# Optimization experiments

Measured on AMD Instinct MI355X. Metric: run time of the kernel, lower is better.

Reference implementation:

```python
import jax, jax.numpy as jnp
import numpy as np
import math

HIDDEN = 1024
HEADS = 16
HEAD_DIM = HIDDEN // HEADS
B, S = 2, 2048


def setup_inputs() -> dict:
    key = jax.random.key(0)
    ks = jax.random.split(key, 10)
    std = 1.0 / math.sqrt(HIDDEN)
    mk = lambda k: (jax.random.normal(k, (HIDDEN, HIDDEN), jnp.float32) * std)
    return {
        "hidden_states": jax.random.normal(ks[0], (B, S, HIDDEN), jnp.float32),
        "attention_mask": jnp.zeros((B, 1, 1, S), jnp.float32),
        "wq": mk(ks[1]), "bq": jnp.zeros((HIDDEN,), jnp.float32),
        "wk": mk(ks[2]), "bk": jnp.zeros((HIDDEN,), jnp.float32),
        "wv": mk(ks[3]), "bv": jnp.zeros((HIDDEN,), jnp.float32),
        "wo": mk(ks[4]), "bo": jnp.zeros((HIDDEN,), jnp.float32),
    }


def reference(hidden_states, attention_mask, wq, bq, wk, bk, wv, bv, wo, bo):
    b, s, _ = hidden_states.shape
    scale = math.sqrt(HEAD_DIM)
    # projections (torch Linear: x @ W.T + b); weights stored as [out, in]
    q = hidden_states @ wq.T + bq
    k = hidden_states @ wk.T + bk
    v = hidden_states @ wv.T + bv
    # [B, H, S, D]
    q = q.reshape(b, s, HEADS, HEAD_DIM).transpose(0, 2, 1, 3)
    k = k.reshape(b, s, HEADS, HEAD_DIM).transpose(0, 2, 1, 3)
    v = v.reshape(b, s, HEADS, HEAD_DIM).transpose(0, 2, 1, 3)
    scores = jnp.einsum("bhqd,bhkd->bhqk", q, k) / scale
    scores = scores + attention_mask  # broadcast [B,1,1,S]
    weights = jax.nn.softmax(scores, axis=-1)  # dropout = identity (eval)
    out = jnp.einsum("bhqk,bhkd->bhqd", weights, v)
    out = out.transpose(0, 2, 1, 3).reshape(b, s, HIDDEN)
    out = out @ wo.T + bo
    return out
```

## Files before the change

kernel.cpp:

```cpp
#include <hip/hip_runtime.h>
#include <hip/hip_bf16.h>

typedef __bf16 bf16_t;
typedef __bf16 bf16x8 __attribute__((ext_vector_type(8)));
typedef _Float16 f16x4 __attribute__((ext_vector_type(4)));
typedef _Float16 f16x8 __attribute__((ext_vector_type(8)));
typedef float f32x4 __attribute__((ext_vector_type(4)));

#define SEQ    2048
#define NH     16
#define HD     64
#define HIDDEN 1024
#define LOG2E  1.44269504f
#define CSTR   41

__device__ __forceinline__ bf16_t to_bf16(float f) { return (bf16_t)f; }

__device__ __forceinline__ void async16(const void* g, void* l) {
    __builtin_amdgcn_global_load_lds((const __attribute__((address_space(1))) void*)g,
                                     (__attribute__((address_space(3))) void*)l, 16, 0, 0);
}

__global__ __launch_bounds__(256) void cvt_kernel(
    const float* __restrict__ s0, bf16_t* __restrict__ d0, int c0,
    const float* __restrict__ s1, bf16_t* __restrict__ d1, int c1,
    const float* __restrict__ s2, bf16_t* __restrict__ d2, int c2,
    const float* __restrict__ s3, bf16_t* __restrict__ d3, int c3,
    const float* __restrict__ s4, bf16_t* __restrict__ d4, int c4)
{
    int blk = blockIdx.x;
    const float* s; bf16_t* d;
    if (blk < c0)              { s = s0; d = d0; }
    else if ((blk -= c0) < c1) { s = s1; d = d1; }
    else if ((blk -= c1) < c2) { s = s2; d = d2; }
    else if ((blk -= c2) < c3) { s = s3; d = d3; }
    else                       { blk -= c3; s = s4; d = d4; }
    const size_t base = (size_t)blk * 2048 + threadIdx.x * 8;
    const float4 a = *(const float4*)&s[base];
    const float4 b = *(const float4*)&s[base + 4];
    bf16x8 o;
    o[0] = (bf16_t)a.x; o[1] = (bf16_t)a.y; o[2] = (bf16_t)a.z; o[3] = (bf16_t)a.w;
    o[4] = (bf16_t)b.x; o[5] = (bf16_t)b.y; o[6] = (bf16_t)b.z; o[7] = (bf16_t)b.w;
    *(bf16x8*)&d[base] = o;
}

__global__ __launch_bounds__(256, 3) void qkv_kernel(
    const bf16_t* __restrict__ X,
    const bf16_t* __restrict__ wq, const bf16_t* __restrict__ wk, const bf16_t* __restrict__ wv,
    const float* __restrict__ bq, const float* __restrict__ bk, const float* __restrict__ bv,
    bf16_t* __restrict__ qws, bf16_t* __restrict__ kws, _Float16* __restrict__ vws)
{
    __shared__ __align__(16) bf16_t Sh[2 * 128 * 64];
    bf16_t* As = Sh;
    bf16_t* Bs = Sh + 128 * 64;
    const int z = blockIdx.z;
    const bf16_t* Wsel = (z == 0) ? wq : (z == 1) ? wk : wv;
    const float*  bsel = (z == 0) ? bq : (z == 1) ? bk : bv;
    const int m0 = blockIdx.y * 128, n0 = blockIdx.x * 128;

    const int t = threadIdx.x, lane = t & 63, w = t >> 6;
    const int w0 = w & 1, w1 = w >> 1, l15 = lane & 15, q4 = lane >> 4;

    f32x4 acc[4][4];
#pragma unroll
    for (int i = 0; i < 4; i++)
#pragma unroll
        for (int j = 0; j < 4; j++) acc[i][j] = f32x4{0.f, 0.f, 0.f, 0.f};

    for (int kt = 0; kt < HIDDEN; kt += 64) {
#pragma unroll
        for (int j = 0; j < 4; j++) {
            const int s = j * 256 + t;
            const int row = s >> 3, c = (s & 7) ^ (row & 7);
            const int lbase = (j * 256 + w * 64) * 8;
            async16(&X[(size_t)(m0 + row) * HIDDEN + kt + c * 8], &As[lbase]);
            async16(&Wsel[(size_t)(n0 + row) * HIDDEN + kt + c * 8], &Bs[lbase]);
        }
        __syncthreads();
#pragma unroll
        for (int ks = 0; ks < 2; ks++) {
            bf16x8 af[4];
#pragma unroll
            for (int ti = 0; ti < 4; ti++) {
                const int ra = w0 * 64 + ti * 16 + l15;
                af[ti] = *(const bf16x8*)&As[ra * 64 + (((ks * 4 + q4) ^ (ra & 7))) * 8];
            }
#pragma unroll
            for (int tj = 0; tj < 4; tj++) {
                const int rb = w1 * 64 + tj * 16 + l15;
                const bf16x8 bfr = *(const bf16x8*)&Bs[rb * 64 + (((ks * 4 + q4) ^ (rb & 7))) * 8];
#pragma unroll
                for (int ti = 0; ti < 4; ti++)
                    acc[ti][tj] = __builtin_amdgcn_mfma_f32_16x16x32_bf16(af[ti], bfr, acc[ti][tj], 0, 0, 0);
            }
        }
        __syncthreads();
    }

    if (z < 2) {
#pragma unroll
        for (int tj = 0; tj < 4; tj++) {
            const int n = w1 * 64 + tj * 16 + l15;
            const float bb = bsel[n0 + n];
            const int ch = (n >> 3), sub = n & 7;
#pragma unroll
            for (int ti = 0; ti < 4; ti++)
#pragma unroll
                for (int r = 0; r < 4; r++) {
                    const int m = w0 * 64 + ti * 16 + q4 * 4 + r;
                    Sh[m * 128 + ((ch ^ (m & 15)) << 3) + sub] = to_bf16(acc[ti][tj][r] + bb);
                }
        }
        __syncthreads();
        bf16_t* dst = (z == 0) ? qws : kws;
#pragma unroll
        for (int i = 0; i < 8; i++) {
            const int g = i * 256 + t;
            const int row = g >> 4, c = g & 15;
            const bf16x8 vv = *(const bf16x8*)&Sh[row * 128 + ((c ^ (row & 15)) << 3)];
            *(bf16x8*)&dst[(size_t)(m0 + row) * HIDDEN + n0 + c * 8] = vv;
        }
    } else {
        _Float16* Vt = (_Float16*)Sh;
#pragma unroll
        for (int tj = 0; tj < 4; tj++) {
            const int n = w1 * 64 + tj * 16 + l15;
            const float bb = bsel[n0 + n];
#pragma unroll
            for (int ti = 0; ti < 4; ti++) {
                const int mb = w0 * 64 + ti * 16 + q4 * 4;
                f16x4 v;
#pragma unroll
                for (int r = 0; r < 4; r++) v[r] = (_Float16)(acc[ti][tj][r] + bb);
                *(f16x4*)&Vt[n * 128 + (((mb >> 3) ^ (n & 15)) << 3) + (mb & 7)] = v;
            }
        }
        __syncthreads();
        const int b = m0 >> 11, sbase = m0 & (SEQ - 1);
#pragma unroll
        for (int i = 0; i < 8; i++) {
            const int g = i * 256 + t;
            const int row = g >> 4, c = g & 15;
            const f16x8 vv = *(const f16x8*)&Vt[row * 128 + ((c ^ (row & 15)) << 3)];
            const int d = (n0 + row) & 63, hh = (n0 + row) >> 6;
            *(f16x8*)&vws[(((size_t)b * NH + hh) * HD + d) * SEQ + sbase + c * 8] = vv;
        }
    }
}

__global__ __launch_bounds__(256, 4) void attn_kernel(
    const bf16_t* __restrict__ Qw, const bf16_t* __restrict__ Kw,
    const _Float16* __restrict__ Vtw, const float* __restrict__ Mask,
    bf16_t* __restrict__ Ow)
{
    __shared__ __align__(16) bf16_t Tiles[2][2][64 * 64];

    const int t = threadIdx.x, lane = t & 63, w = t >> 6;
    const int l15 = lane & 15, q4 = lane >> 4;
    const int wq = w & 1, kh = w >> 1;
    const int lid = blockIdx.x;
    const int c8 = lid & 7, j = lid >> 3;
    const int bh = c8 * 4 + (j >> 5);
    const int q0 = (j & 31) * 64;
    const int b = bh >> 4, h = bh & 15;

    const bf16_t* Qh = Qw + (size_t)b * SEQ * HIDDEN + h * HD;
    const bf16_t* Kh = Kw + (size_t)b * SEQ * HIDDEN + h * HD;
    const _Float16* Vh = Vtw + (size_t)bh * HD * SEQ;
    const float* Mrow = Mask + (size_t)b * SEQ;

    bf16x8 qf[2][2];
#pragma unroll
    for (int nq = 0; nq < 2; nq++)
#pragma unroll
        for (int ks = 0; ks < 2; ks++)
            qf[nq][ks] = *(const bf16x8*)&Qh[(size_t)(q0 + wq * 32 + nq * 16 + l15) * HIDDEN + ks * 32 + q4 * 8];

    f32x4 oacc[2][4];
#pragma unroll
    for (int nq = 0; nq < 2; nq++)
#pragma unroll
        for (int nb = 0; nb < 4; nb++) oacc[nq][nb] = f32x4{0.f, 0.f, 0.f, 0.f};
    f32x4 pacc[2] = {f32x4{0.f, 0.f, 0.f, 0.f}, f32x4{0.f, 0.f, 0.f, 0.f}};
    const f16x4 vones = {(_Float16)1.f, (_Float16)1.f, (_Float16)1.f, (_Float16)1.f};

    bf16_t* Ksh = &Tiles[kh][0][0];
    _Float16* Vsh = (_Float16*)&Tiles[kh][1][0];
    const int kbase = kh * (SEQ / 2);

    for (int it = 0; it < 16; it++) {
        const int kt = kbase + it * 64;
#pragma unroll
        for (int jj = 0; jj < 4; jj++) {
            const int s = jj * 128 + wq * 64 + lane;
            const int row = s >> 3, c = (s & 7) ^ (row & 7);
            const int lbase = (jj * 128 + wq * 64) * 8;
            async16(&Kh[(size_t)(kt + row) * HIDDEN + c * 8], &Ksh[lbase]);
            async16(&Vh[(size_t)row * SEQ + kt + c * 8], &Vsh[lbase]);
        }
        __syncthreads();

        f32x4 sa[2][4];
#pragma unroll
        for (int nq = 0; nq < 2; nq++)
#pragma unroll
            for (int cb = 0; cb < 4; cb++) sa[nq][cb] = f32x4{0.f, 0.f, 0.f, 0.f};
#pragma unroll
        for (int cb = 0; cb < 4; cb++)
#pragma unroll
            for (int ks = 0; ks < 2; ks++) {
                const int rk = cb * 16 + l15;
                const bf16x8 kf = *(const bf16x8*)&Ksh[rk * 64 + (((ks * 4 + q4) ^ (rk & 7))) * 8];
                sa[0][cb] = __builtin_amdgcn_mfma_f32_16x16x32_bf16(kf, qf[0][ks], sa[0][cb], 0, 0, 0);
                sa[1][cb] = __builtin_amdgcn_mfma_f32_16x16x32_bf16(kf, qf[1][ks], sa[1][cb], 0, 0, 0);
            }

        f16x4 ph[2][4];
#pragma unroll
        for (int cb = 0; cb < 4; cb++) {
            float4 mv = *(const float4*)&Mrow[kt + cb * 16 + q4 * 4];
            mv.x *= LOG2E; mv.y *= LOG2E; mv.z *= LOG2E; mv.w *= LOG2E;
            const float mk[4] = {mv.x, mv.y, mv.z, mv.w};
#pragma unroll
            for (int nq = 0; nq < 2; nq++) {
#pragma unroll
                for (int r = 0; r < 4; r++)
                    ph[nq][cb][r] = (_Float16)exp2f(fmaf(sa[nq][cb][r], 0.125f * LOG2E, mk[r]));
            }
        }

#pragma unroll
        for (int cb = 0; cb < 4; cb++) {
#pragma unroll
            for (int nb = 0; nb < 4; nb++) {
                const int rv = nb * 16 + l15;
                const int cl = (cb * 2 + (q4 >> 1)) ^ (rv & 7);
                const f16x4 vf = *(const f16x4*)&Vsh[rv * 64 + cl * 8 + (q4 & 1) * 4];
                oacc[0][nb] = __builtin_amdgcn_mfma_f32_16x16x16f16(ph[0][cb], vf, oacc[0][nb], 0, 0, 0);
                oacc[1][nb] = __builtin_amdgcn_mfma_f32_16x16x16f16(ph[1][cb], vf, oacc[1][nb], 0, 0, 0);
            }
            pacc[0] = __builtin_amdgcn_mfma_f32_16x16x16f16(ph[0][cb], vones, pacc[0], 0, 0, 0);
            pacc[1] = __builtin_amdgcn_mfma_f32_16x16x16f16(ph[1][cb], vones, pacc[1], 0, 0, 0);
        }
        __syncthreads();
    }

    float* Cb = (float*)&Tiles[0][0][0];
    const int crow = (wq * 64 + lane) * CSTR;
    if (kh == 1) {
#pragma unroll
        for (int nq = 0; nq < 2; nq++) {
#pragma unroll
            for (int nb = 0; nb < 4; nb++)
                *(f32x4*)&Cb[crow + (nq * 5 + nb) * 4] = oacc[nq][nb];
            *(f32x4*)&Cb[crow + (nq * 5 + 4) * 4] = pacc[nq];
        }
    }
    __syncthreads();
    if (kh == 0) {
#pragma unroll
        for (int nq = 0; nq < 2; nq++) {
#pragma unroll
            for (int nb = 0; nb < 4; nb++)
                oacc[nq][nb] += *(const f32x4*)&Cb[crow + (nq * 5 + nb) * 4];
            pacc[nq] += *(const f32x4*)&Cb[crow + (nq * 5 + 4) * 4];
        }
#pragma unroll
        for (int nq = 0; nq < 2; nq++)
#pragma unroll
            for (int r = 0; r < 4; r++) {
                const float inv = 1.f / pacc[nq][r];
                const int s = q0 + wq * 32 + nq * 16 + q4 * 4 + r;
#pragma unroll
                for (int nb = 0; nb < 4; nb++)
                    Ow[((size_t)b * SEQ + s) * HIDDEN + h * HD + nb * 16 + l15] =
                        to_bf16(oacc[nq][nb][r] * inv);
            }
    }
}

__global__ __launch_bounds__(256, 2) void oproj_kernel(
    const bf16_t* __restrict__ A, const bf16_t* __restrict__ Wo,
    const float* __restrict__ bo, float* __restrict__ Out)
{
    __shared__ __align__(16) bf16_t As[64 * 64];
    __shared__ __align__(16) bf16_t Bs[128 * 64];
    const int m0 = blockIdx.y * 64, n0 = blockIdx.x * 128;
    const int t = threadIdx.x, lane = t & 63, w = t >> 6;
    const int l15 = lane & 15, q4 = lane >> 4;

    f32x4 acc[4][2];
#pragma unroll
    for (int i = 0; i < 4; i++)
#pragma unroll
        for (int j = 0; j < 2; j++) acc[i][j] = f32x4{0.f, 0.f, 0.f, 0.f};

    for (int kt = 0; kt < HIDDEN; kt += 64) {
#pragma unroll
        for (int j = 0; j < 2; j++) {
            const int s = j * 256 + t;
            const int row = s >> 3, c = (s & 7) ^ (row & 7);
            async16(&A[(size_t)(m0 + row) * HIDDEN + kt + c * 8], &As[(j * 256 + w * 64) * 8]);
        }
#pragma unroll
        for (int j = 0; j < 4; j++) {
            const int s = j * 256 + t;
            const int row = s >> 3, c = (s & 7) ^ (row & 7);
            async16(&Wo[(size_t)(n0 + row) * HIDDEN + kt + c * 8], &Bs[(j * 256 + w * 64) * 8]);
        }
        __syncthreads();
#pragma unroll
        for (int ks = 0; ks < 2; ks++) {
            bf16x8 af[4];
#pragma unroll
            for (int ti = 0; ti < 4; ti++) {
                const int ra = ti * 16 + l15;
                af[ti] = *(const bf16x8*)&As[ra * 64 + (((ks * 4 + q4) ^ (ra & 7))) * 8];
            }
#pragma unroll
            for (int tj = 0; tj < 2; tj++) {
                const int rb = w * 32 + tj * 16 + l15;
                const bf16x8 bfr = *(const bf16x8*)&Bs[rb * 64 + (((ks * 4 + q4) ^ (rb & 7))) * 8];
#pragma unroll
                for (int ti = 0; ti < 4; ti++)
                    acc[ti][tj] = __builtin_amdgcn_mfma_f32_16x16x32_bf16(bfr, af[ti], acc[ti][tj], 0, 0, 0);
            }
        }
        __syncthreads();
    }

#pragma unroll
    for (int tj = 0; tj < 2; tj++) {
        const int nb4 = n0 + w * 32 + tj * 16 + q4 * 4;
        const float4 bb = *(const float4*)&bo[nb4];
#pragma unroll
        for (int ti = 0; ti < 4; ti++) {
            const int m = m0 + ti * 16 + l15;
            float4 ov;
            ov.x = acc[ti][tj][0] + bb.x;
            ov.y = acc[ti][tj][1] + bb.y;
            ov.z = acc[ti][tj][2] + bb.z;
            ov.w = acc[ti][tj][3] + bb.w;
            *(float4*)&Out[(size_t)m * HIDDEN + nb4] = ov;
        }
    }
}

extern "C" void kernel_launch(void* const* d_in, const int* in_sizes, int n_in,
                              void* d_out, int out_size, void* d_ws, size_t ws_size,
                              hipStream_t stream) {
    const float* X   = (const float*)d_in[0];
    const float* msk = (const float*)d_in[1];
    const float* wq  = (const float*)d_in[2];
    const float* bq  = (const float*)d_in[3];
    const float* wk  = (const float*)d_in[4];
    const float* bk  = (const float*)d_in[5];
    const float* wv  = (const float*)d_in[6];
    const float* bv  = (const float*)d_in[7];
    const float* wo  = (const float*)d_in[8];
    const float* bo  = (const float*)d_in[9];
    float* out = (float*)d_out;

    const size_t NELT = (size_t)2 * SEQ * HIDDEN;
    const size_t WELT = (size_t)HIDDEN * HIDDEN;
    bf16_t*    xbf = (bf16_t*)d_ws;
    bf16_t*    qws = xbf + NELT;
    bf16_t*    kws = qws + NELT;
    _Float16*  vws = (_Float16*)(kws + NELT);
    bf16_t*    aws = xbf;
    bf16_t*    wqb = (bf16_t*)d_out;
    bf16_t*    wkb = wqb + WELT;
    bf16_t*    wvb = wkb + WELT;
    bf16_t*    wob = wvb + WELT;

    cvt_kernel<<<dim3(2048 + 4 * 512), dim3(256), 0, stream>>>(
        X, xbf, 2048, wq, wqb, 512, wk, wkb, 512, wv, wvb, 512, wo, wob, 512);
    qkv_kernel<<<dim3(8, 32, 3), dim3(256), 0, stream>>>(
        xbf, wqb, wkb, wvb, bq, bk, bv, qws, kws, vws);
    attn_kernel<<<dim3(1024), dim3(256), 0, stream>>>(qws, kws, vws, msk, aws);
    oproj_kernel<<<dim3(8, 64), dim3(256), 0, stream>>>(aws, wob, bo, out);
}
```

Baseline: 208.7 us.

## Double-buffer GEMM K-tiles and replace MFMA row-sum with scalar softmax sums

The QKV and output-projection GEMMs now use two 32-wide K-tile buffers in the same shared memory footprint. Each iteration prefetches the next tile with async loads while computing on the current one, using one barrier per iteration instead of two, which is meant to hide global load latency. The attention kernel drops the extra MFMA against a ones vector that computed softmax denominators. It accumulates row sums in scalar registers and reduces them with lane shuffles instead, cutting MFMA work at the cost of extra VALU adds and shuffles.

New measurement: 208.4 us. About the same (-0.1%).

```diff
diff --git a/kernel.cpp b/kernel.cpp
--- a/kernel.cpp
+++ b/kernel.cpp
@@ -50,9 +50,7 @@
     const float* __restrict__ bq, const float* __restrict__ bk, const float* __restrict__ bv,
     bf16_t* __restrict__ qws, bf16_t* __restrict__ kws, _Float16* __restrict__ vws)
 {
-    __shared__ __align__(16) bf16_t Sh[2 * 128 * 64];
-    bf16_t* As = Sh;
-    bf16_t* Bs = Sh + 128 * 64;
+    __shared__ __align__(16) bf16_t Sh[16384];
     const int z = blockIdx.z;
     const bf16_t* Wsel = (z == 0) ? wq : (z == 1) ? wk : wv;
     const float*  bsel = (z == 0) ? bq : (z == 1) ? bk : bv;
@@ -67,35 +65,40 @@
 #pragma unroll
         for (int j = 0; j < 4; j++) acc[i][j] = f32x4{0.f, 0.f, 0.f, 0.f};
 
-    for (int kt = 0; kt < HIDDEN; kt += 64) {
-#pragma unroll
-        for (int j = 0; j < 4; j++) {
+    auto stage = [&](int kt, int buf) {
+#pragma unroll
+        for (int j = 0; j < 2; j++) {
             const int s = j * 256 + t;
-            const int row = s >> 3, c = (s & 7) ^ (row & 7);
-            const int lbase = (j * 256 + w * 64) * 8;
-            async16(&X[(size_t)(m0 + row) * HIDDEN + kt + c * 8], &As[lbase]);
-            async16(&Wsel[(size_t)(n0 + row) * HIDDEN + kt + c * 8], &Bs[lbase]);
-        }
-        __syncthreads();
-#pragma unroll
-        for (int ks = 0; ks < 2; ks++) {
-            bf16x8 af[4];
-#pragma unroll
-            for (int ti = 0; ti < 4; ti++) {
-                const int ra = w0 * 64 + ti * 16 + l15;
-                af[ti] = *(const bf16x8*)&As[ra * 64 + (((ks * 4 + q4) ^ (ra & 7))) * 8];
-            }
-#pragma unroll
-            for (int tj = 0; tj < 4; tj++) {
-                const int rb = w1 * 64 + tj * 16 + l15;
-                const bf16x8 bfr = *(const bf16x8*)&Bs[rb * 64 + (((ks * 4 + q4) ^ (rb & 7))) * 8];
-#pragma unroll
-                for (int ti = 0; ti < 4; ti++)
-                    acc[ti][tj] = __builtin_amdgcn_mfma_f32_16x16x32_bf16(af[ti], bfr, acc[ti][tj], 0, 0, 0);
-            }
-        }
-        __syncthreads();
-    }
+            const int row = s >> 2, c = (s & 3) ^ (row & 3);
+            const int lb = buf * 8192 + (j * 256 + w * 64) * 8;
+            async16(&X[(size_t)(m0 + row) * HIDDEN + kt + c * 8], &Sh[lb]);
+            async16(&Wsel[(size_t)(n0 + row) * HIDDEN + kt + c * 8], &Sh[lb + 4096]);
+        }
+    };
+    stage(0, 0);
+
+    for (int it = 0; it < 32; it++) {
+        const int cur = it & 1;
+        __syncthreads();
+        if (it < 31) stage((it + 1) * 32, cur ^ 1);
+        const bf16_t* As = &Sh[cur * 8192];
+        const bf16_t* Bs = &Sh[cur * 8192 + 4096];
+        bf16x8 af[4];
+#pragma unroll
+        for (int ti = 0; ti < 4; ti++) {
+            const int ra = w0 * 64 + ti * 16 + l15;
+            af[ti] = *(const bf16x8*)&As[ra * 32 + (q4 ^ (ra & 3)) * 8];
+        }
+#pragma unroll
+        for (int tj = 0; tj < 4; tj++) {
+            const int rb = w1 * 64 + tj * 16 + l15;
+            const bf16x8 bfr = *(const bf16x8*)&Bs[rb * 32 + (q4 ^ (rb & 3)) * 8];
+#pragma unroll
+            for (int ti = 0; ti < 4; ti++)
+                acc[ti][tj] = __builtin_amdgcn_mfma_f32_16x16x32_bf16(af[ti], bfr, acc[ti][tj], 0, 0, 0);
+        }
+    }
+    __syncthreads();
 
     if (z < 2) {
 #pragma unroll
@@ -181,18 +184,18 @@
     for (int nq = 0; nq < 2; nq++)
 #pragma unroll
         for (int nb = 0; nb < 4; nb++) oacc[nq][nb] = f32x4{0.f, 0.f, 0.f, 0.f};
-    f32x4 pacc[2] = {f32x4{0.f, 0.f, 0.f, 0.f}, f32x4{0.f, 0.f, 0.f, 0.f}};
-    const f16x4 vones = {(_Float16)1.f, (_Float16)1.f, (_Float16)1.f, (_Float16)1.f};
+    float psum[2] = {0.f, 0.f};
 
     bf16_t* Ksh = &Tiles[kh][0][0];
     _Float16* Vsh = (_Float16*)&Tiles[kh][1][0];
     const int kbase = kh * (SEQ / 2);
+    const int s0_ = wq * 64 + lane;
 
     for (int it = 0; it < 16; it++) {
         const int kt = kbase + it * 64;
 #pragma unroll
         for (int jj = 0; jj < 4; jj++) {
-            const int s = jj * 128 + wq * 64 + lane;
+            const int s = jj * 128 + s0_;
             const int row = s >> 3, c = (s & 7) ^ (row & 7);
             const int lbase = (jj * 128 + wq * 64) * 8;
             async16(&Kh[(size_t)(kt + row) * HIDDEN + c * 8], &Ksh[lbase]);
@@ -224,8 +227,11 @@
 #pragma unroll
             for (int nq = 0; nq < 2; nq++) {
 #pragma unroll
-                for (int r = 0; r < 4; r++)
-                    ph[nq][cb][r] = (_Float16)exp2f(fmaf(sa[nq][cb][r], 0.125f * LOG2E, mk[r]));
+                for (int r = 0; r < 4; r++) {
+                    const float p = exp2f(fmaf(sa[nq][cb][r], 0.125f * LOG2E, mk[r]));
+                    psum[nq] += p;
+                    ph[nq][cb][r] = (_Float16)p;
+                }
             }
         }
 
@@ -239,10 +245,14 @@
                 oacc[0][nb] = __builtin_amdgcn_mfma_f32_16x16x16f16(ph[0][cb], vf, oacc[0][nb], 0, 0, 0);
                 oacc[1][nb] = __builtin_amdgcn_mfma_f32_16x16x16f16(ph[1][cb], vf, oacc[1][nb], 0, 0, 0);
             }
-            pacc[0] = __builtin_amdgcn_mfma_f32_16x16x16f16(ph[0][cb], vones, pacc[0], 0, 0, 0);
-            pacc[1] = __builtin_amdgcn_mfma_f32_16x16x16f16(ph[1][cb], vones, pacc[1], 0, 0, 0);
-        }
-        __syncthreads();
+        }
+        __syncthreads();
+    }
+
+#pragma unroll
+    for (int nq = 0; nq < 2; nq++) {
+        psum[nq] += __shfl_xor(psum[nq], 16);
+        psum[nq] += __shfl_xor(psum[nq], 32);
     }
 
     float* Cb = (float*)&Tiles[0][0][0];
@@ -252,8 +262,8 @@
         for (int nq = 0; nq < 2; nq++) {
 #pragma unroll
             for (int nb = 0; nb < 4; nb++)
-                *(f32x4*)&Cb[crow + (nq * 5 + nb) * 4] = oacc[nq][nb];
-            *(f32x4*)&Cb[crow + (nq * 5 + 4) * 4] = pacc[nq];
+                *(f32x4*)&Cb[crow + (nq * 4 + nb) * 4] = oacc[nq][nb];
+            Cb[crow + 32 + nq] = psum[nq];
         }
     }
     __syncthreads();
@@ -262,20 +272,23 @@
         for (int nq = 0; nq < 2; nq++) {
 #pragma unroll
             for (int nb = 0; nb < 4; nb++)
-                oacc[nq][nb] += *(const f32x4*)&Cb[crow + (nq * 5 + nb) * 4];
-            pacc[nq] += *(const f32x4*)&Cb[crow + (nq * 5 + 4) * 4];
-        }
-#pragma unroll
-        for (int nq = 0; nq < 2; nq++)
+                oacc[nq][nb] += *(const f32x4*)&Cb[crow + (nq * 4 + nb) * 4];
+            psum[nq] += Cb[crow + 32 + nq];
+        }
+#pragma unroll
+        for (int nq = 0; nq < 2; nq++) {
+            float inv[4];
+#pragma unroll
+            for (int r = 0; r < 4; r++) inv[r] = 1.f / __shfl(psum[nq], q4 * 4 + r);
 #pragma unroll
             for (int r = 0; r < 4; r++) {
-                const float inv = 1.f / pacc[nq][r];
                 const int s = q0 + wq * 32 + nq * 16 + q4 * 4 + r;
 #pragma unroll
                 for (int nb = 0; nb < 4; nb++)
                     Ow[((size_t)b * SEQ + s) * HIDDEN + h * HD + nb * 16 + l15] =
-                        to_bf16(oacc[nq][nb][r] * inv);
-            }
+                        to_bf16(oacc[nq][nb][r] * inv[r]);
+            }
+        }
     }
 }
 
@@ -283,8 +296,7 @@
     const bf16_t* __restrict__ A, const bf16_t* __restrict__ Wo,
     const float* __restrict__ bo, float* __restrict__ Out)
 {
-    __shared__ __align__(16) bf16_t As[64 * 64];
-    __shared__ __align__(16) bf16_t Bs[128 * 64];
+    __shared__ __align__(16) bf16_t Sh[12288];
     const int m0 = blockIdx.y * 64, n0 = blockIdx.x * 128;
     const int t = threadIdx.x, lane = t & 63, w = t >> 6;
     const int l15 = lane & 15, q4 = lane >> 4;
@@ -295,38 +307,41 @@
 #pragma unroll
         for (int j = 0; j < 2; j++) acc[i][j] = f32x4{0.f, 0.f, 0.f, 0.f};
 
-    for (int kt = 0; kt < HIDDEN; kt += 64) {
+    auto stage = [&](int kt, int buf) {
+        {
+            const int row = t >> 2, c = (t & 3) ^ (row & 3);
+            async16(&A[(size_t)(m0 + row) * HIDDEN + kt + c * 8], &Sh[buf * 6144 + w * 64 * 8]);
+        }
 #pragma unroll
         for (int j = 0; j < 2; j++) {
             const int s = j * 256 + t;
-            const int row = s >> 3, c = (s & 7) ^ (row & 7);
-            async16(&A[(size_t)(m0 + row) * HIDDEN + kt + c * 8], &As[(j * 256 + w * 64) * 8]);
-        }
-#pragma unroll
-        for (int j = 0; j < 4; j++) {
-            const int s = j * 256 + t;
-            const int row = s >> 3, c = (s & 7) ^ (row & 7);
-            async16(&Wo[(size_t)(n0 + row) * HIDDEN + kt + c * 8], &Bs[(j * 256 + w * 64) * 8]);
-        }
-        __syncthreads();
-#pragma unroll
-        for (int ks = 0; ks < 2; ks++) {
-            bf16x8 af[4];
-#pragma unroll
-            for (int ti = 0; ti < 4; ti++) {
-                const int ra = ti * 16 + l15;
-                af[ti] = *(const bf16x8*)&As[ra * 64 + (((ks * 4 + q4) ^ (ra & 7))) * 8];
-            }
-#pragma unroll
-            for (int tj = 0; tj < 2; tj++) {
-                const int rb = w * 32 + tj * 16 + l15;
-                const bf16x8 bfr = *(const bf16x8*)&Bs[rb * 64 + (((ks * 4 + q4) ^ (rb & 7))) * 8];
-#pragma unroll
-                for (int ti = 0; ti < 4; ti++)
-                    acc[ti][tj] = __builtin_amdgcn_mfma_f32_16x16x32_bf16(bfr, af[ti], acc[ti][tj], 0, 0, 0);
-            }
-        }
-        __syncthreads();
+            const int row = s >> 2, c = (s & 3) ^ (row & 3);
+            async16(&Wo[(size_t)(n0 + row) * HIDDEN + kt + c * 8],
+                    &Sh[buf * 6144 + 2048 + (j * 256 + w * 64) * 8]);
+        }
+    };
+    stage(0, 0);
+
+    for (int it = 0; it < 32; it++) {
+        const int cur = it & 1;
+        __syncthreads();
+        if (it < 31) stage((it + 1) * 32, cur ^ 1);
+        const bf16_t* As = &Sh[cur * 6144];
+        const bf16_t* Bs = &Sh[cur * 6144 + 2048];
+        bf16x8 af[4];
+#pragma unroll
+        for (int ti = 0; ti < 4; ti++) {
+            const int ra = ti * 16 + l15;
+            af[ti] = *(const bf16x8*)&As[ra * 32 + (q4 ^ (ra & 3)) * 8];
+        }
+#pragma unroll
+        for (int tj = 0; tj < 2; tj++) {
+            const int rb = w * 32 + tj * 16 + l15;
+            const bf16x8 bfr = *(const bf16x8*)&Bs[rb * 32 + (q4 ^ (rb & 3)) * 8];
+#pragma unroll
+            for (int ti = 0; ti < 4; ti++)
+                acc[ti][tj] = __builtin_amdgcn_mfma_f32_16x16x32_bf16(bfr, af[ti], acc[ti][tj], 0, 0, 0);
+        }
     }
 
 #pragma unroll
```
